# Kernel tuning notes

Measured on AMD Instinct MI355X. Metric: run time of the kernel, lower is better.

Reference implementation:

```python
import jax, jax.numpy as jnp
import numpy as np

N = 32768       # nodes
DEG = 8         # incoming edges per node (plus 1 self loop added by GCNConv)
HID = 128       # hidden_dim
WID = 128       # network_width (== hidden_dim, required by residual)
ND = 9          # SelfAttnAggregation.node_degree
AD = WID + ND   # attention embed dim = 137


def setup_inputs() -> dict:
    key = jax.random.key(0)
    ks = jax.random.split(key, 12)
    x = jax.random.normal(ks[0], (N, HID + 2), dtype=jnp.float32)
    # fixed in-degree graph: each node has DEG random incoming edges
    src = jax.random.randint(ks[1], (N * DEG,), 0, N, dtype=jnp.int32)
    dst = jnp.repeat(jnp.arange(N, dtype=jnp.int32), DEG)
    edge_index = jnp.stack([src, dst])
    s = 0.1
    return {
        "x": x,
        "edge_index": edge_index,
        "W1": jax.random.normal(ks[2], (HID + 2, WID), jnp.float32) * s,
        "b1": jax.random.normal(ks[3], (WID,), jnp.float32) * s,
        "W2": jax.random.normal(ks[4], (WID, WID), jnp.float32) * s,
        "b2": jax.random.normal(ks[5], (WID,), jnp.float32) * s,
        # [conv(2), attn(2), qkv(3), AD, AD] — torch MultiheadAttention in_proj
        "qkv_w": jax.random.normal(ks[6], (2, 2, 3, AD, AD), jnp.float32) * s,
        "qkv_b": jax.random.normal(ks[7], (2, 2, 3, AD), jnp.float32) * s,
        "out_w": jax.random.normal(ks[8], (2, 2, AD, AD), jnp.float32) * s,
        "out_b": jax.random.normal(ks[9], (2, 2, AD), jnp.float32) * s,
    }


def _mha(d, wqkv, bqkv, wo, bo):
    # d: [N, ND, AD]; single-head torch MultiheadAttention (q=k=v=d)
    q = jnp.einsum("nsd,ed->nse", d, wqkv[0]) + bqkv[0]
    k = jnp.einsum("nsd,ed->nse", d, wqkv[1]) + bqkv[1]
    v = jnp.einsum("nsd,ed->nse", d, wqkv[2]) + bqkv[2]
    scores = jnp.einsum("nqe,nke->nqk", q, k) / np.sqrt(AD).astype(np.float32)
    a = jax.nn.softmax(scores, axis=-1)
    o = jnp.einsum("nqk,nke->nqe", a, v)
    return jnp.einsum("nse,oe->nso", o, wo) + bo


def _gcn_attn_conv(h_in, W, b, neighbors, qkv_w, qkv_b, out_w, out_b):
    # GCNConv(normalize=False): lin -> gather messages -> SelfAttnAggregation -> +bias
    h = h_in @ W                                   # [N, WID]
    m = h[neighbors]                               # [N, ND, WID] irregular gather
    pos = jnp.broadcast_to(jnp.eye(ND, dtype=h.dtype), (N, ND, ND))
    d = jnp.concatenate([m, pos], axis=-1)         # [N, ND, AD]
    y = d + _mha(d, qkv_w[0], qkv_b[0], out_w[0], out_b[0]) \
          + _mha(d, qkv_w[1], qkv_b[1], out_w[1], out_b[1])
    return jnp.max(y[..., :WID], axis=1) + b       # [N, WID]


def _pairnorm(h):
    h = h - jnp.mean(h, axis=0, keepdims=True)
    denom = jnp.sqrt(1e-6 + jnp.mean(jnp.sum(h * h, axis=-1)))
    return h / denom


def reference(x, edge_index, W1, b1, W2, b2, qkv_w, qkv_b, out_w, out_b):
    src = edge_index[0]
    # [N, ND] neighbor table: DEG incoming sources + self loop (add_self_loops=True)
    nbr = jnp.concatenate(
        [src.reshape(N, DEG), jnp.arange(N, dtype=src.dtype)[:, None]], axis=1
    )
    u = _gcn_attn_conv(x, W1, b1, nbr, qkv_w[0], qkv_b[0], out_w[0], out_b[0])
    u = jax.nn.relu(_pairnorm(u))
    u = _gcn_attn_conv(u, W2, b2, nbr, qkv_w[1], qkv_b[1], out_w[1], out_b[1])
    u = jax.nn.relu(_pairnorm(u))
    x2 = x[:, :-2] + u                             # [N, HID]
    last = x2[:, -1]
    last = jnp.where((last > 1.0) | (last < -1.0), jnp.float32(0.0), last)
    return x2.at[:, -1].set(last) / 2.0
```

## Files before the change

kernel.cpp:

```cpp
#include <hip/hip_runtime.h>
#include <hip/hip_bf16.h>

#define NN 32768
#define DEG 8
#define PW 548
#define GW 676
#define TP 428

typedef unsigned short u16;
typedef unsigned int u32;

__device__ __forceinline__ float bf2f(u32 lo16) { return __uint_as_float(lo16 << 16); }

__global__ void detect_kernel(const void* __restrict__ x, int* __restrict__ flagp) {
  if (threadIdx.x == 0) {
    const u16* u = (const u16*)x;
    int insane = 0;
    for (int i = 0; i < 128; ++i) {
      int e = (u[i] >> 7) & 0xff;
      if (e == 0 || e == 0xff || e < 0x70 || e > 0x8f) insane++;
    }
    *flagp = (insane >= 16) ? 0 : 1;
  }
}

struct CvtAll {
  const void* src[9];
  float* dst[9];
  int cum[10];
};

__global__ void cvt_all_kernel(CvtAll d, const int* __restrict__ flagp) {
  const int f = *flagp;
  const int total = d.cum[9];
  for (int g = blockIdx.x * 256 + threadIdx.x; g < total; g += gridDim.x * 256) {
    int s = 0;
    #pragma unroll
    for (int k = 1; k < 9; ++k) s += (g >= d.cum[k]);
    const int i = g - d.cum[s];
    if (f) d.dst[s][i] = bf2f((u32)((const u16*)d.src[s])[i]);
    else   d.dst[s][i] = ((const float*)d.src[s])[i];
  }
}

__global__ __launch_bounds__(256) void derive_small_kernel(
    const float* __restrict__ qw, const float* __restrict__ qb,
    const float* __restrict__ ow, const float* __restrict__ ob,
    float* __restrict__ cq, float* __restrict__ ck, float* __restrict__ cvo,
    float* __restrict__ cc, float* __restrict__ bo_sum) {
  const int hd = blockIdx.x;
  const float* Wq = qw + (size_t)(hd*3 + 0) * 18769;
  const float* Wk = qw + (size_t)(hd*3 + 1) * 18769;
  const float* Wv = qw + (size_t)(hd*3 + 2) * 18769;
  const float* bq = qb + (hd*3 + 0) * 137;
  const float* bk = qb + (hd*3 + 1) * 137;
  const float* bv = qb + (hd*3 + 2) * 137;
  const float* Wo = ow + (size_t)hd * 18769;
  const int tid = threadIdx.x;

  for (int idx = tid; idx < 9*137; idx += 256) {
    int s = idx / 137, e = idx % 137;
    cq[hd*1233 + idx] = Wq[e*137 + 128 + s] + bq[e];
    ck[hd*1233 + idx] = Wk[e*137 + 128 + s] + bk[e];
  }
  __syncthreads();

  for (int idx = tid; idx < 9*128; idx += 256) {
    int s = idx >> 7, oi = idx & 127;
    float a = 0.f;
    for (int e = 0; e < 137; ++e) a += Wo[oi*137 + e] * (Wv[e*137 + 128 + s] + bv[e]);
    cvo[hd*1152 + idx] = a;
  }
  for (int idx = tid; idx < 81; idx += 256) {
    int i = idx / 9, j = idx % 9;
    float a = 0.f;
    for (int e = 0; e < 137; ++e) a += cq[hd*1233 + i*137 + e] * ck[hd*1233 + j*137 + e];
    cc[hd*81 + idx] = a;
  }
  if ((hd & 1) == 0) {
    int l = hd >> 1;
    for (int oi = tid; oi < 128; oi += 256)
      bo_sum[l*128 + oi] = ob[(l*2 + 0)*137 + oi] + ob[(l*2 + 1)*137 + oi];
  }
}

__global__ __launch_bounds__(256) void derive_mm_kernel(
    const float* __restrict__ qw, const float* __restrict__ ow,
    float* __restrict__ Mqk, float* __restrict__ Mvo) {
  const int hd = blockIdx.y;
  const float* Wq = qw + (size_t)(hd*3 + 0) * 18769;
  const float* Wk = qw + (size_t)(hd*3 + 1) * 18769;
  const float* Wv = qw + (size_t)(hd*3 + 2) * 18769;
  const float* Wo = ow + (size_t)hd * 18769;
  const int idx = blockIdx.x * 256 + threadIdx.x;
  const int row = idx >> 7, col = idx & 127;
  float sq = 0.f, so = 0.f;
  #pragma unroll 4
  for (int e = 0; e < 137; ++e) {
    sq += Wq[e*137 + row] * Wk[e*137 + col];
    so += Wo[row*137 + e] * Wv[e*137 + col];
  }
  Mqk[hd*16384 + idx] = sq;
  Mvo[hd*16384 + idx] = so;
}

__global__ void bigw_kernel(const float* __restrict__ qw,
                            const float* __restrict__ Mqk, const float* __restrict__ Mvo,
                            const float* __restrict__ cq, const float* __restrict__ ck,
                            float* __restrict__ BigW) {
  const int idx = blockIdx.x * 256 + threadIdx.x;
  if (idx >= 2 * 128 * PW) return;
  const int l = idx / (128 * PW);
  const int r = idx % (128 * PW);
  const int k = r / PW, col = r % PW;
  float v = 0.f;
  if (col < 128)       v = Mqk[(l*2 + 0)*16384 + k*128 + col];
  else if (col < 256)  v = Mqk[(l*2 + 1)*16384 + k*128 + (col - 128)];
  else if (col < 274) {
    int q = col - 256, t = q / 9, j = q % 9;
    const float* Wq = qw + (size_t)((l*2 + t)*3 + 0) * 18769;
    const float* ckp = ck + (l*2 + t)*1233 + j*137;
    float a = 0.f;
    for (int e = 0; e < 137; ++e) a += Wq[e*137 + k] * ckp[e];
    v = a;
  } else if (col < 292) {
    int q = col - 274, t = q / 9, i = q % 9;
    const float* Wk_ = qw + (size_t)((l*2 + t)*3 + 1) * 18769;
    const float* cqp = cq + (l*2 + t)*1233 + i*137;
    float a = 0.f;
    for (int e = 0; e < 137; ++e) a += cqp[e] * Wk_[e*137 + k];
    v = a;
  }
  else if (col < 420)  v = Mvo[(l*2 + 0)*16384 + (col - 292)*128 + k];
  else                 v = Mvo[(l*2 + 1)*16384 + (col - 420)*128 + k];
  BigW[idx] = v;
}

__global__ __launch_bounds__(256) void buildb_kernel(
    const float* __restrict__ W1, const float* __restrict__ W2,
    const float* __restrict__ BigW, float* __restrict__ BigB) {
  const int l = blockIdx.y;
  const int Kl = l ? 128 : 130;
  const float* W = l ? W2 : W1;
  const int idx = blockIdx.x * 256 + threadIdx.x;
  if (idx >= Kl * 676) return;
  const int k = idx / 676, c = idx % 676;
  float v;
  if (c < 128) {
    v = W[k * 128 + c];
  } else {
    const int c2 = c - 128;
    const float* Wk = W + k * 128;
    const float* Bc = BigW + (size_t)l * 128 * PW + c2;
    float a = 0.f;
    #pragma unroll 4
    for (int m = 0; m < 128; ++m) a += Wk[m] * Bc[(size_t)m * PW];
    v = a;
  }
  BigB[(size_t)l * 130 * 676 + (size_t)k * 676 + c] = v;
}

__global__ __launch_bounds__(256) void gemm128_kernel(
    const float* __restrict__ A, const float* __restrict__ B,
    float* __restrict__ C,
    int M, int K, int NC, int lda, int ldb, int ldc,
    const float* __restrict__ astats) {
  __shared__ float As[16][128];
  __shared__ float Bs[16][132];
  const int tid = threadIdx.x;
  const int row0 = blockIdx.y * 128, col0 = blockIdx.x * 128;
  const int tx = tid & 15, ty = tid >> 4;
  const float ainv = astats ? astats[128] : 1.f;
  const int ar = tid >> 1, aq = (tid & 1) * 8;
  const int bk = tid >> 4, bc = (tid & 15) * 8;
  float av[8], bv[8];
  float acc[8][8] = {};
  const int nsteps = (K + 15) / 16;

  auto loadA = [&](int k0) {
    const float* Ap = A + (size_t)(row0 + ar) * lda + k0 + aq;
    if (k0 + 16 <= K) {
      const float4 v0 = *(const float4*)Ap;
      const float4 v1 = *(const float4*)(Ap + 4);
      av[0]=v0.x; av[1]=v0.y; av[2]=v0.z; av[3]=v0.w;
      av[4]=v1.x; av[5]=v1.y; av[6]=v1.z; av[7]=v1.w;
    } else {
      #pragma unroll
      for (int p = 0; p < 8; ++p) av[p] = (k0 + aq + p < K) ? Ap[p] : 0.f;
    }
    if (astats) {
      #pragma unroll
      for (int p = 0; p < 8; ++p) {
        const int kc = k0 + aq + p;
        if (kc < K) av[p] = fmaxf((av[p] - astats[kc]) * ainv, 0.f);
      }
    }
  };
  auto loadB = [&](int k0) {
    const int kg = k0 + bk;
    const float* Bp = B + (size_t)kg * ldb + col0 + bc;
    if (kg < K && col0 + bc + 8 <= NC) {
      const float4 v0 = *(const float4*)Bp;
      const float4 v1 = *(const float4*)(Bp + 4);
      bv[0]=v0.x; bv[1]=v0.y; bv[2]=v0.z; bv[3]=v0.w;
      bv[4]=v1.x; bv[5]=v1.y; bv[6]=v1.z; bv[7]=v1.w;
    } else {
      #pragma unroll
      for (int p = 0; p < 8; ++p)
        bv[p] = (kg < K && col0 + bc + p < NC) ? Bp[p] : 0.f;
    }
  };

  loadA(0); loadB(0);
  for (int step = 0; step < nsteps; ++step) {
    #pragma unroll
    for (int p = 0; p < 8; ++p) As[aq + p][ar] = av[p];
    *(float4*)&Bs[bk][bc]     = make_float4(bv[0], bv[1], bv[2], bv[3]);
    *(float4*)&Bs[bk][bc + 4] = make_float4(bv[4], bv[5], bv[6], bv[7]);
    __syncthreads();
    if (step + 1 < nsteps) { loadA((step + 1) * 16); loadB((step + 1) * 16); }
    #pragma unroll
    for (int kk = 0; kk < 16; ++kk) {
      float a[8], b[8];
      *(float4*)&a[0] = *(const float4*)&As[kk][ty * 8];
      *(float4*)&a[4] = *(const float4*)&As[kk][ty * 8 + 4];
      *(float4*)&b[0] = *(const float4*)&Bs[kk][tx * 8];
      *(float4*)&b[4] = *(const float4*)&Bs[kk][tx * 8 + 4];
      #pragma unroll
      for (int i = 0; i < 8; ++i)
        #pragma unroll
        for (int j = 0; j < 8; ++j)
          acc[i][j] += a[i] * b[j];
    }
    __syncthreads();
  }
  #pragma unroll
  for (int i = 0; i < 8; ++i) {
    const int rr = row0 + ty * 8 + i;
    float* Cp = C + (size_t)rr * ldc + col0 + tx * 8;
    if (col0 + tx * 8 + 8 <= NC) {
      *(float4*)Cp       = make_float4(acc[i][0], acc[i][1], acc[i][2], acc[i][3]);
      *(float4*)(Cp + 4) = make_float4(acc[i][4], acc[i][5], acc[i][6], acc[i][7]);
    } else {
      #pragma unroll
      for (int j = 0; j < 8; ++j)
        if (col0 + tx * 8 + j < NC) Cp[j] = acc[i][j];
    }
  }
}

__global__ __launch_bounds__(256) void attn_kernel(
    const int* __restrict__ src, const float* __restrict__ G,
    const float* __restrict__ cvo, const float* __restrict__ cc,
    const float* __restrict__ bo_sum, const float* __restrict__ b_layer,
    int layer, float* __restrict__ res) {
  __shared__ float T[9][TP];
  __shared__ float As[2][9][9];
  __shared__ float ymax[2][128];
  __shared__ int nbr[9];
  const int n = blockIdx.x;
  const int tid = threadIdx.x;
  if (tid < 9) nbr[tid] = (tid < 8) ? src[n * DEG + tid] : n;
  __syncthreads();
  for (int it = tid; it < 9 * 105; it += 256) {
    const int s = it / 105, w = it % 105;
    *(float4*)&T[s][w * 4] = *(const float4*)(G + (size_t)nbr[s] * GW + w * 4);
  }
  __syncthreads();
  if (tid < 162) {
    const int t = tid / 81, r = tid % 81, i = r / 9, j = r % 9;
    const float* hm = &T[i][128 + t * 128];
    const float* hj = &T[j][0];
    float s = 0.f;
    #pragma unroll 8
    for (int c = 0; c < 128; c += 4) {
      const float4 a = *(const float4*)&hm[c];
      const float4 b = *(const float4*)&hj[c];
      s += a.x * b.x + a.y * b.y + a.z * b.z + a.w * b.w;
    }
    s += T[i][384 + t*9 + j] + T[j][402 + t*9 + i] + cc[(layer*2 + t)*81 + r];
    As[t][i][j] = s * 0.08543576577f;
  }
  __syncthreads();
  if (tid < 18) {
    const int t = tid / 9, i = tid % 9;
    float* row = &As[t][i][0];
    float m = -3e38f;
    #pragma unroll
    for (int j = 0; j < 9; ++j) m = fmaxf(m, row[j]);
    float ex[9], ssum = 0.f;
    #pragma unroll
    for (int j = 0; j < 9; ++j) { ex[j] = expf(row[j] - m); ssum += ex[j]; }
    const float inv = 1.f / ssum;
    #pragma unroll
    for (int j = 0; j < 9; ++j) row[j] = ex[j] * inv;
  }
  __syncthreads();
  {
    const int oi = tid & 127, half = tid >> 7;
    const float* cvo1 = cvo + (layer * 2 + 0) * 1152 + oi;
    const float* cvo2 = cvo + (layer * 2 + 1) * 1152 + oi;
    float vg1[9], vg2[9];
    #pragma unroll
    for (int j = 0; j < 9; ++j) {
      const float* gr = G + (size_t)nbr[j] * GW + oi;
      vg1[j] = gr[420] + cvo1[j * 128];
      vg2[j] = gr[548] + cvo2[j * 128];
    }
    float mx = -3e38f;
    const int i0 = half ? 5 : 0, i1 = half ? 9 : 5;
    for (int i = i0; i < i1; ++i) {
      float y = T[i][oi];
      #pragma unroll
      for (int j = 0; j < 9; ++j)
        y += As[0][i][j] * vg1[j] + As[1][i][j] * vg2[j];
      mx = fmaxf(mx, y);
    }
    ymax[half][oi] = mx;
  }
  __syncthreads();
  if (tid < 128) {
    const float v = fmaxf(ymax[0][tid], ymax[1][tid]) + bo_sum[layer*128 + tid] + b_layer[tid];
    res[(size_t)n * 128 + tid] = v;
  }
}

__global__ __launch_bounds__(256) void reduce_kernel(const float* __restrict__ res,
                                                     float* __restrict__ partial) {
  __shared__ float col2[128];
  __shared__ float sqs[256];
  const int b = blockIdx.x, tid = threadIdx.x;
  const int c = tid & 127, half = tid >> 7;
  float cs = 0.f, sq = 0.f;
  const int r0 = half * 64;
  for (int r = r0; r < r0 + 64; ++r) {
    const float v = res[((size_t)b * 128 + r) * 128 + c];
    cs += v; sq += v * v;
  }
  if (half) col2[c] = cs;
  sqs[tid] = sq;
  __syncthreads();
  if (!half) partial[b * 129 + c] = cs + col2[c];
  for (int s = 128; s >= 1; s >>= 1) {
    if (tid < s) sqs[tid] += sqs[tid + s];
    __syncthreads();
  }
  if (tid == 0) partial[b * 129 + 128] = sqs[0];
}

__global__ __launch_bounds__(1024) void finalize_kernel(const float* __restrict__ partial,
                                                        float* __restrict__ stats) {
  __shared__ float colsum[8][128];
  __shared__ float sqred[256];
  __shared__ float musq[128];
  const int tid = threadIdx.x;
  const int c = tid & 127, g = tid >> 7;
  float cs = 0.f;
  #pragma unroll 8
  for (int b = g * 32; b < g * 32 + 32; ++b) cs += partial[b * 129 + c];
  colsum[g][c] = cs;
  if (tid < 256) sqred[tid] = partial[tid * 129 + 128];
  __syncthreads();
  if (tid < 128) {
    float m = 0.f;
    #pragma unroll
    for (int g2 = 0; g2 < 8; ++g2) m += colsum[g2][tid];
    m *= (1.f / 32768.f);
    stats[tid] = m;
    musq[tid] = m * m;
  }
  __syncthreads();
  for (int s = 128; s >= 1; s >>= 1) {
    if (tid < s) sqred[tid] += sqred[tid + s];
    if (s <= 64 && tid < s) musq[tid] += musq[tid + s];
    __syncthreads();
  }
  if (tid == 0) {
    const float var = sqred[0] * (1.f / 32768.f) - musq[0];
    stats[128] = 1.f / sqrtf(1e-6f + var);
  }
}

__global__ void final_kernel(const float* __restrict__ res, const float* __restrict__ stats,
                             const float* __restrict__ xf, void* __restrict__ out,
                             const int* __restrict__ flagp) {
  const int idx = blockIdx.x * 256 + threadIdx.x;
  const int nrow = idx >> 7, c = idx & 127;
  float v = fmaxf((res[idx] - stats[c]) * stats[128], 0.f);
  v += xf[(size_t)nrow * 130 + c];
  if (c == 127 && (v > 1.f || v < -1.f)) v = 0.f;
  v *= 0.5f;
  if (*flagp) ((__hip_bfloat16*)out)[idx] = __float2bfloat16(v);
  else        ((float*)out)[idx] = v;
}

extern "C" void kernel_launch(void* const* d_in, const int* in_sizes, int n_in,
                              void* d_out, int out_size, void* d_ws, size_t ws_size,
                              hipStream_t stream) {
  (void)in_sizes; (void)n_in; (void)out_size; (void)ws_size;
  char* ws = (char*)d_ws;
  size_t off = 0;
  auto alloc = [&](size_t bytes) -> char* {
    char* p = ws + off;
    off += (bytes + 255) & ~(size_t)255;
    return p;
  };
  int*   flagp = (int*)  alloc(4);
  float* xf    = (float*)alloc((size_t)NN * 130 * 4);
  float* W1f   = (float*)alloc(130 * 128 * 4);
  float* b1f   = (float*)alloc(128 * 4);
  float* W2f   = (float*)alloc(128 * 128 * 4);
  float* b2f   = (float*)alloc(128 * 4);
  float* qwf   = (float*)alloc((size_t)225228 * 4);
  float* qbf   = (float*)alloc(1644 * 4);
  float* owf   = (float*)alloc((size_t)75076 * 4);
  float* obf   = (float*)alloc(548 * 4);
  float* Mqk   = (float*)alloc((size_t)4 * 16384 * 4);
  float* Mvo   = (float*)alloc((size_t)4 * 16384 * 4);
  float* cq    = (float*)alloc((size_t)4 * 1233 * 4);
  float* ck    = (float*)alloc((size_t)4 * 1233 * 4);
  float* cvo   = (float*)alloc((size_t)4 * 1152 * 4);
  float* cc    = (float*)alloc((size_t)4 * 81 * 4);
  float* boS   = (float*)alloc((size_t)2 * 128 * 4);
  float* BigW  = (float*)alloc((size_t)2 * 128 * PW * 4);
  float* BigB  = (float*)alloc((size_t)2 * 130 * 676 * 4);
  float* G     = (float*)alloc((size_t)NN * GW * 4);
  float* res   = (float*)alloc((size_t)NN * 128 * 4);
  float* part  = (float*)alloc((size_t)256 * 129 * 4);
  float* st0   = (float*)alloc(132 * 4);
  float* st1   = (float*)alloc(132 * 4);

  const int* edge = (const int*)d_in[1];

  detect_kernel<<<1, 64, 0, stream>>>(d_in[0], flagp);

  CvtAll ca;
  {
    const int srcidx[9] = {0, 2, 3, 4, 5, 6, 7, 8, 9};
    float* dsts[9] = {xf, W1f, b1f, W2f, b2f, qwf, qbf, owf, obf};
    const int ns[9] = {NN * 130, 130 * 128, 128, 128 * 128, 128,
                       225228, 1644, 75076, 548};
    int acc = 0;
    for (int i = 0; i < 9; ++i) {
      ca.src[i] = d_in[srcidx[i]];
      ca.dst[i] = dsts[i];
      ca.cum[i] = acc;
      acc += ns[i];
    }
    ca.cum[9] = acc;
  }
  cvt_all_kernel<<<4096, 256, 0, stream>>>(ca, flagp);

  derive_small_kernel<<<4, 256, 0, stream>>>(qwf, qbf, owf, obf, cq, ck, cvo, cc, boS);
  derive_mm_kernel<<<dim3(64, 4), 256, 0, stream>>>(qwf, owf, Mqk, Mvo);
  bigw_kernel<<<(2 * 128 * PW + 255) / 256, 256, 0, stream>>>(qwf, Mqk, Mvo, cq, ck, BigW);
  buildb_kernel<<<dim3((130 * 676 + 255) / 256, 2), 256, 0, stream>>>(W1f, W2f, BigW, BigB);

  for (int l = 0; l < 2; ++l) {
    const float* act = l ? res : xf;
    const int K = l ? 128 : 130;
    gemm128_kernel<<<dim3((GW + 127) / 128, NN / 128), 256, 0, stream>>>(
        act, BigB + (size_t)l * 130 * 676, G,
        NN, K, GW, K, 676, GW, l ? st0 : nullptr);
    attn_kernel<<<NN, 256, 0, stream>>>(edge, G, cvo, cc, boS,
                                        l ? b2f : b1f, l, res);
    reduce_kernel<<<256, 256, 0, stream>>>(res, part);
    finalize_kernel<<<1, 1024, 0, stream>>>(part, l ? st1 : st0);
  }
  final_kernel<<<NN * 128 / 256, 256, 0, stream>>>(res, st1, xf, d_out, flagp);
}
```

Baseline: 650.2 us.

## Split GEMM into full-tile main kernel plus narrow tail kernel, pad x rows

```diff
diff --git a/kernel.cpp b/kernel.cpp
--- a/kernel.cpp
+++ b/kernel.cpp
@@ -6,6 +6,7 @@
 #define PW 548
 #define GW 676
 #define TP 428
+#define XW 132
 
 typedef unsigned short u16;
 typedef unsigned int u32;
@@ -38,49 +39,52 @@
     #pragma unroll
     for (int k = 1; k < 9; ++k) s += (g >= d.cum[k]);
     const int i = g - d.cum[s];
-    if (f) d.dst[s][i] = bf2f((u32)((const u16*)d.src[s])[i]);
-    else   d.dst[s][i] = ((const float*)d.src[s])[i];
-  }
-}
-
-__global__ __launch_bounds__(256) void derive_small_kernel(
+    float v;
+    if (f) v = bf2f((u32)((const u16*)d.src[s])[i]);
+    else   v = ((const float*)d.src[s])[i];
+    if (s == 0) d.dst[0][(i / 130) * XW + (i % 130)] = v;
+    else        d.dst[s][i] = v;
+  }
+}
+
+__global__ __launch_bounds__(256) void derive_cqck_kernel(
+    const float* __restrict__ qw, const float* __restrict__ qb,
+    float* __restrict__ cq, float* __restrict__ ck) {
+  const int hd = blockIdx.y;
+  const float* Wq = qw + (size_t)(hd*3 + 0) * 18769;
+  const float* Wk = qw + (size_t)(hd*3 + 1) * 18769;
+  const float* bq = qb + (hd*3 + 0) * 137;
+  const float* bk = qb + (hd*3 + 1) * 137;
+  const int idx = blockIdx.x * 256 + threadIdx.x;
+  if (idx >= 1233) return;
+  const int s = idx / 137, e = idx % 137;
+  cq[hd*1233 + idx] = Wq[e*137 + 128 + s] + bq[e];
+  ck[hd*1233 + idx] = Wk[e*137 + 128 + s] + bk[e];
+}
+
+__global__ __launch_bounds__(256) void derive_rest_kernel(
     const float* __restrict__ qw, const float* __restrict__ qb,
     const float* __restrict__ ow, const float* __restrict__ ob,
-    float* __restrict__ cq, float* __restrict__ ck, float* __restrict__ cvo,
-    float* __restrict__ cc, float* __restrict__ bo_sum) {
-  const int hd = blockIdx.x;
-  const float* Wq = qw + (size_t)(hd*3 + 0) * 18769;
-  const float* Wk = qw + (size_t)(hd*3 + 1) * 18769;
+    const float* __restrict__ cq, const float* __restrict__ ck,
+    float* __restrict__ cvo, float* __restrict__ cc, float* __restrict__ bo_sum) {
+  const int hd = blockIdx.y;
   const float* Wv = qw + (size_t)(hd*3 + 2) * 18769;
-  const float* bq = qb + (hd*3 + 0) * 137;
-  const float* bk = qb + (hd*3 + 1) * 137;
   const float* bv = qb + (hd*3 + 2) * 137;
   const float* Wo = ow + (size_t)hd * 18769;
-  const int tid = threadIdx.x;
-
-  for (int idx = tid; idx < 9*137; idx += 256) {
-    int s = idx / 137, e = idx % 137;
-    cq[hd*1233 + idx] = Wq[e*137 + 128 + s] + bq[e];
-    ck[hd*1233 + idx] = Wk[e*137 + 128 + s] + bk[e];
-  }
-  __syncthreads();
-
-  for (int idx = tid; idx < 9*128; idx += 256) {
-    int s = idx >> 7, oi = idx & 127;
+  const int idx = blockIdx.x * 256 + threadIdx.x;
+  if (idx < 1152) {
+    const int s = idx >> 7, oi = idx & 127;
     float a = 0.f;
     for (int e = 0; e < 137; ++e) a += Wo[oi*137 + e] * (Wv[e*137 + 128 + s] + bv[e]);
     cvo[hd*1152 + idx] = a;
-  }
-  for (int idx = tid; idx < 81; idx += 256) {
-    int i = idx / 9, j = idx % 9;
+  } else if (idx < 1233) {
+    const int r = idx - 1152, i = r / 9, j = r % 9;
     float a = 0.f;
     for (int e = 0; e < 137; ++e) a += cq[hd*1233 + i*137 + e] * ck[hd*1233 + j*137 + e];
-    cc[hd*81 + idx] = a;
-  }
-  if ((hd & 1) == 0) {
-    int l = hd >> 1;
-    for (int oi = tid; oi < 128; oi += 256)
-      bo_sum[l*128 + oi] = ob[(l*2 + 0)*137 + oi] + ob[(l*2 + 1)*137 + oi];
+    cc[hd*81 + r] = a;
+  } else if (idx < 1361 && (hd & 1) == 0) {
+    const int oi = idx - 1233, l = hd >> 1;
+    bo_sum[l*128 + oi] = ob[(l*2 + 0)*137 + oi] + ob[(l*2 + 1)*137 + oi];
   }
 }
 
@@ -160,7 +164,7 @@
   BigB[(size_t)l * 130 * 676 + (size_t)k * 676 + c] = v;
 }
 
-__global__ __launch_bounds__(256) void gemm128_kernel(
+__global__ __launch_bounds__(256, 5) void gemm128_kernel(
     const float* __restrict__ A, const float* __restrict__ B,
     float* __restrict__ C,
     int M, int K, int NC, int lda, int ldb, int ldc,
@@ -173,12 +177,14 @@
   const float ainv = astats ? astats[128] : 1.f;
   const int ar = tid >> 1, aq = (tid & 1) * 8;
   const int bk = tid >> 4, bc = (tid & 15) * 8;
+  const float* Arow = A + (size_t)(row0 + ar) * lda + aq;
+  const float* Bcol = B + (size_t)bk * ldb + col0 + bc;
   float av[8], bv[8];
   float acc[8][8] = {};
   const int nsteps = (K + 15) / 16;
 
   auto loadA = [&](int k0) {
-    const float* Ap = A + (size_t)(row0 + ar) * lda + k0 + aq;
+    const float* Ap = Arow + k0;
     if (k0 + 16 <= K) {
       const float4 v0 = *(const float4*)Ap;
       const float4 v1 = *(const float4*)(Ap + 4);
@@ -198,16 +204,15 @@
   };
   auto loadB = [&](int k0) {
     const int kg = k0 + bk;
-    const float* Bp = B + (size_t)kg * ldb + col0 + bc;
-    if (kg < K && col0 + bc + 8 <= NC) {
+    const float* Bp = Bcol + (size_t)k0 * ldb;
+    if (kg < K) {
       const float4 v0 = *(const float4*)Bp;
       const float4 v1 = *(const float4*)(Bp + 4);
       bv[0]=v0.x; bv[1]=v0.y; bv[2]=v0.z; bv[3]=v0.w;
       bv[4]=v1.x; bv[5]=v1.y; bv[6]=v1.z; bv[7]=v1.w;
     } else {
       #pragma unroll
-      for (int p = 0; p < 8; ++p)
-        bv[p] = (kg < K && col0 + bc + p < NC) ? Bp[p] : 0.f;
+      for (int p = 0; p < 8; ++p) bv[p] = 0.f;
     }
   };
 
@@ -238,15 +243,64 @@
   for (int i = 0; i < 8; ++i) {
     const int rr = row0 + ty * 8 + i;
     float* Cp = C + (size_t)rr * ldc + col0 + tx * 8;
-    if (col0 + tx * 8 + 8 <= NC) {
-      *(float4*)Cp       = make_float4(acc[i][0], acc[i][1], acc[i][2], acc[i][3]);
-      *(float4*)(Cp + 4) = make_float4(acc[i][4], acc[i][5], acc[i][6], acc[i][7]);
-    } else {
-      #pragma unroll
-      for (int j = 0; j < 8; ++j)
-        if (col0 + tx * 8 + j < NC) Cp[j] = acc[i][j];
-    }
-  }
+    *(float4*)Cp       = make_float4(acc[i][0], acc[i][1], acc[i][2], acc[i][3]);
+    *(float4*)(Cp + 4) = make_float4(acc[i][4], acc[i][5], acc[i][6], acc[i][7]);
+  }
+}
+
+__global__ __launch_bounds__(256) void gemm_tail_kernel(
+    const float* __restrict__ A, const float* __restrict__ B,
+    float* __restrict__ C,
+    int K, int NC0, int lda, int ldb, int ldc,
+    const float* __restrict__ astats) {
+  __shared__ float As[16][128];
+  __shared__ float Bs[16][36];
+  const int tid = threadIdx.x;
+  const int row0 = blockIdx.x * 128;
+  const int r = tid >> 1, g = tid & 1;
+  const int aq = g * 8;
+  const float ainv = astats ? astats[128] : 1.f;
+  const float* Arow = A + (size_t)(row0 + r) * lda + aq;
+  float acc[18] = {};
+  for (int k0 = 0; k0 < K; k0 += 16) {
+    {
+      const float* Ap = Arow + k0;
+      float av[8];
+      if (k0 + 16 <= K) {
+        const float4 v0 = *(const float4*)Ap;
+        const float4 v1 = *(const float4*)(Ap + 4);
+        av[0]=v0.x; av[1]=v0.y; av[2]=v0.z; av[3]=v0.w;
+        av[4]=v1.x; av[5]=v1.y; av[6]=v1.z; av[7]=v1.w;
+      } else {
+        #pragma unroll
+        for (int p = 0; p < 8; ++p) av[p] = (k0 + aq + p < K) ? Ap[p] : 0.f;
+      }
+      if (astats) {
+        #pragma unroll
+        for (int p = 0; p < 8; ++p) {
+          const int kc = k0 + aq + p;
+          if (kc < K) av[p] = fmaxf((av[p] - astats[kc]) * ainv, 0.f);
+        }
+      }
+      #pragma unroll
+      for (int p = 0; p < 8; ++p) As[aq + p][r] = av[p];
+    }
+    for (int idx = tid; idx < 16 * 36; idx += 256) {
+      const int kk = idx / 36, c = idx % 36;
+      Bs[kk][c] = (k0 + kk < K) ? B[(size_t)(k0 + kk) * ldb + NC0 + c] : 0.f;
+    }
+    __syncthreads();
+    #pragma unroll
+    for (int kk = 0; kk < 16; ++kk) {
+      const float a = As[kk][r];
+      #pragma unroll
+      for (int c = 0; c < 18; ++c) acc[c] += a * Bs[kk][g * 18 + c];
+    }
+    __syncthreads();
+  }
+  float* Cp = C + (size_t)(row0 + r) * ldc + NC0 + g * 18;
+  #pragma unroll
+  for (int c = 0; c < 18; ++c) Cp[c] = acc[c];
 }
 
 __global__ __launch_bounds__(256) void attn_kernel(
@@ -387,7 +441,7 @@
   const int idx = blockIdx.x * 256 + threadIdx.x;
   const int nrow = idx >> 7, c = idx & 127;
   float v = fmaxf((res[idx] - stats[c]) * stats[128], 0.f);
-  v += xf[(size_t)nrow * 130 + c];
+  v += xf[(size_t)nrow * XW + c];
   if (c == 127 && (v > 1.f || v < -1.f)) v = 0.f;
   v *= 0.5f;
   if (*flagp) ((__hip_bfloat16*)out)[idx] = __float2bfloat16(v);
@@ -406,7 +460,7 @@
     return p;
   };
   int*   flagp = (int*)  alloc(4);
-  float* xf    = (float*)alloc((size_t)NN * 130 * 4);
+  float* xf    = (float*)alloc((size_t)NN * XW * 4);
   float* W1f   = (float*)alloc(130 * 128 * 4);
   float* b1f   = (float*)alloc(128 * 4);
   float* W2f   = (float*)alloc(128 * 128 * 4);
@@ -451,7 +505,9 @@
   }
   cvt_all_kernel<<<4096, 256, 0, stream>>>(ca, flagp);
 
-  derive_small_kernel<<<4, 256, 0, stream>>>(qwf, qbf, owf, obf, cq, ck, cvo, cc, boS);
+  derive_cqck_kernel<<<dim3(5, 4), 256, 0, stream>>>(qwf, qbf, cq, ck);
+  derive_rest_kernel<<<dim3(6, 4), 256, 0, stream>>>(qwf, qbf, owf, obf, cq, ck,
+                                                     cvo, cc, boS);
   derive_mm_kernel<<<dim3(64, 4), 256, 0, stream>>>(qwf, owf, Mqk, Mvo);
   bigw_kernel<<<(2 * 128 * PW + 255) / 256, 256, 0, stream>>>(qwf, Mqk, Mvo, cq, ck, BigW);
   buildb_kernel<<<dim3((130 * 676 + 255) / 256, 2), 256, 0, stream>>>(W1f, W2f, BigW, BigB);
@@ -459,9 +515,14 @@
   for (int l = 0; l < 2; ++l) {
     const float* act = l ? res : xf;
     const int K = l ? 128 : 130;
-    gemm128_kernel<<<dim3((GW + 127) / 128, NN / 128), 256, 0, stream>>>(
+    const int lda = l ? 128 : XW;
+    const float* st = l ? st0 : nullptr;
+    gemm128_kernel<<<dim3(5, NN / 128), 256, 0, stream>>>(
         act, BigB + (size_t)l * 130 * 676, G,
-        NN, K, GW, K, 676, GW, l ? st0 : nullptr);
+        NN, K, 640, lda, 676, GW, st);
+    gemm_tail_kernel<<<NN / 128, 256, 0, stream>>>(
+        act, BigB + (size_t)l * 130 * 676, G,
+        K, 640, lda, 676, GW, st);
     attn_kernel<<<NN, 256, 0, stream>>>(edge, G, cvo, cc, boS,
                                         l ? b2f : b1f, l, res);
     reduce_kernel<<<256, 256, 0, stream>>>(res, part);
```

New measurement: 2.144 ms. 3.3x slower.
